# Optimization experiments

Measured on AMD Instinct MI355X. Metric: run time of the kernel, lower is better.

Reference implementation:

```python
import jax, jax.numpy as jnp
import numpy as np

B, T, D, H = 256, 1024, 128, 128

def setup_inputs() -> dict:
    key = jax.random.key(0)
    k1, k2, k3, k4 = jax.random.split(key, 4)
    return {
        "x": jax.random.normal(k1, (B, T, D), dtype=jnp.float32),
        "w": jax.random.normal(k2, (D, H), dtype=jnp.float32) * 0.05,
        "state_weight": jax.random.normal(k3, (H, H), dtype=jnp.float32) * 0.05,
        "b": jax.random.normal(k4, (H,), dtype=jnp.float32) * 0.05,
    }

def reference(x, w, state_weight, b):
    # Faithful Elman RNN with return_sequences=False.
    # Original transposes input to time-major [T, B, D], initializes the
    # state from step 0 WITHOUT a recurrent term, then iterates steps 1..T-1.
    X = jnp.transpose(x, (1, 0, 2))  # [T, B, D]
    # Precompute input projections for all steps in one big GEMM (same math).
    proj = jnp.einsum("tbd,dh->tbh", X, w) + b  # [T, B, H]
    state0 = jnp.tanh(proj[0])

    def step(state, pt):
        y = jnp.tanh(pt + state @ state_weight)
        return y, None

    final_state, _ = jax.lax.scan(step, state0, proj[1:])
    return final_state  # [B, H]
```

## Files before the change

### kernel.cpp

```cpp
#include <hip/hip_runtime.h>

#define T_N 1024
#define H_N 128
#define CH   64
#define NCH (T_N / CH)
#define WPAD 136
#define PPAD 68

typedef __attribute__((ext_vector_type(8))) short bf16x8;
typedef __attribute__((ext_vector_type(4))) float f32x4;

__device__ __forceinline__ short f2bf_rne(float f) {
    union { float f; unsigned int i; } v; v.f = f;
    unsigned int r = v.i + 0x7FFFu + ((v.i >> 16) & 1u);
    return (short)(r >> 16);
}

__global__ __launch_bounds__(512, 1) void k_fused(const float* __restrict__ x,
                                                  const float* __restrict__ w,
                                                  const float* __restrict__ wst,
                                                  const float* __restrict__ bias,
                                                  float* __restrict__ out) {
    __shared__ __align__(16) short wT[H_N * WPAD];
    __shared__ __align__(16) float pT[H_N * PPAD];
    __shared__ __align__(16) short sst[2][H_N];

    const int tid  = threadIdx.x;
    const int wv   = tid >> 6;
    const int lane = tid & 63;
    const int l = lane & 15;
    const int q = lane >> 4;
    const int tt = wv >> 1;
    const int h  = wv & 1;
    const int r = blockIdx.x;
    const float* xrow = x + (size_t)r * T_N * H_N;
    const f32x4 zero4 = (f32x4){0.f, 0.f, 0.f, 0.f};

    const float* xlane = xrow + (size_t)(tt * 16 + l) * H_N + q * 8;
    float4 xst[8];
    #pragma unroll
    for (int ks = 0; ks < 4; ++ks) {
        xst[ks * 2 + 0] = *reinterpret_cast<const float4*>(xlane + ks * 32);
        xst[ks * 2 + 1] = *reinterpret_cast<const float4*>(xlane + ks * 32 + 4);
    }

    short* wsTs = reinterpret_cast<short*>(pT);
    for (int e = tid * 4; e < H_N * H_N; e += 2048) {
        int k = e >> 7, n = e & 127;
        float4 a4 = *reinterpret_cast<const float4*>(wst + e);
        wsTs[(n + 0) * WPAD + k] = f2bf_rne(a4.x);
        wsTs[(n + 1) * WPAD + k] = f2bf_rne(a4.y);
        wsTs[(n + 2) * WPAD + k] = f2bf_rne(a4.z);
        wsTs[(n + 3) * WPAD + k] = f2bf_rne(a4.w);
    }
    __syncthreads();

    bf16x8 wf[4];
    #pragma unroll
    for (int ks = 0; ks < 4; ++ks)
        wf[ks] = *reinterpret_cast<const bf16x8*>(
            &wsTs[(16 * wv + l) * WPAD + ks * 32 + q * 8]);

    if (tid < 128) sst[0][tid] = 0;

    for (int e = tid * 4; e < H_N * H_N; e += 2048) {
        int k = e >> 7, n = e & 127;
        float4 a4 = *reinterpret_cast<const float4*>(w + e);
        wT[(n + 0) * WPAD + k] = f2bf_rne(a4.x);
        wT[(n + 1) * WPAD + k] = f2bf_rne(a4.y);
        wT[(n + 2) * WPAD + k] = f2bf_rne(a4.z);
        wT[(n + 3) * WPAD + k] = f2bf_rne(a4.w);
    }

    float bv[4];
    #pragma unroll
    for (int j = 0; j < 4; ++j) bv[j] = bias[(4 * h + j) * 16 + l];

    __syncthreads();

    float y = 0.f;
    const int rowp = (16 * wv + l) * PPAD;

    auto step = [&](const short* srd, short* swr, float pv) {
        bf16x8 a0 = *reinterpret_cast<const bf16x8*>(&srd[ 0 + q * 8]);
        bf16x8 a1 = *reinterpret_cast<const bf16x8*>(&srd[32 + q * 8]);
        bf16x8 a2 = *reinterpret_cast<const bf16x8*>(&srd[64 + q * 8]);
        bf16x8 a3 = *reinterpret_cast<const bf16x8*>(&srd[96 + q * 8]);
        f32x4 c4 = (f32x4){pv, pv, pv, pv};
        f32x4 x0 = __builtin_amdgcn_mfma_f32_16x16x32_bf16(a0, wf[0], c4, 0, 0, 0);
        f32x4 x1 = __builtin_amdgcn_mfma_f32_16x16x32_bf16(a1, wf[1], zero4, 0, 0, 0);
        f32x4 x2 = __builtin_amdgcn_mfma_f32_16x16x32_bf16(a2, wf[2], zero4, 0, 0, 0);
        f32x4 x3 = __builtin_amdgcn_mfma_f32_16x16x32_bf16(a3, wf[3], zero4, 0, 0, 0);
        float z = (x0[0] + x1[0]) + (x2[0] + x3[0]);
        float e = __expf(2.0f * z);
        y = __builtin_fmaf(-2.0f, __builtin_amdgcn_rcpf(e + 1.0f), 1.0f);
        unsigned int pk;
        asm("v_cvt_pk_bf16_f32 %0, %1, %2" : "=v"(pk) : "v"(y), "v"(y));
        if (q == 0)
            swr[16 * wv + l] = (short)pk;
        __syncthreads();
    };

    #pragma unroll 1
    for (int c = 0; c < NCH; ++c) {
        bf16x8 ax[4];
        #pragma unroll
        for (int ks = 0; ks < 4; ++ks) {
            float4 u0 = xst[ks * 2 + 0];
            float4 u1 = xst[ks * 2 + 1];
            bf16x8 f;
            f[0] = f2bf_rne(u0.x); f[1] = f2bf_rne(u0.y);
            f[2] = f2bf_rne(u0.z); f[3] = f2bf_rne(u0.w);
            f[4] = f2bf_rne(u1.x); f[5] = f2bf_rne(u1.y);
            f[6] = f2bf_rne(u1.z); f[7] = f2bf_rne(u1.w);
            ax[ks] = f;
        }

        if (c + 1 < NCH) {
            const float* pn = xlane + (size_t)(c + 1) * CH * H_N;
            #pragma unroll
            for (int ks = 0; ks < 4; ++ks) {
                xst[ks * 2 + 0] = *reinterpret_cast<const float4*>(pn + ks * 32);
                xst[ks * 2 + 1] = *reinterpret_cast<const float4*>(pn + ks * 32 + 4);
            }
        }


        #pragma unroll
        for (int j = 0; j < 4; ++j) {
            const int nt = 4 * h + j;
            f32x4 cb = (f32x4){bv[j], bv[j], bv[j], bv[j]};
            f32x4 acc;
            #pragma unroll
            for (int ks = 0; ks < 4; ++ks) {
                bf16x8 bw = *reinterpret_cast<const bf16x8*>(
                    &wT[(nt * 16 + l) * WPAD + ks * 32 + q * 8]);
                acc = __builtin_amdgcn_mfma_f32_16x16x32_bf16(
                    ax[ks], bw, ks == 0 ? cb : acc, 0, 0, 0);
            }
            *reinterpret_cast<f32x4*>(&pT[(nt * 16 + l) * PPAD + tt * 16 + q * 4]) = acc;
        }

        __syncthreads();

        #pragma unroll 1
        for (int s = 0; s < CH / 8; ++s) {
            float4 pb0 = *reinterpret_cast<const float4*>(&pT[rowp + 8 * s]);
            float4 pb1 = *reinterpret_cast<const float4*>(&pT[rowp + 8 * s + 4]);
            step(sst[0], sst[1], pb0.x);
            step(sst[1], sst[0], pb0.y);
            step(sst[0], sst[1], pb0.z);
            step(sst[1], sst[0], pb0.w);
            step(sst[0], sst[1], pb1.x);
            step(sst[1], sst[0], pb1.y);
            step(sst[0], sst[1], pb1.z);
            step(sst[1], sst[0], pb1.w);
        }
    }

    if (q == 0)
        out[r * H_N + 16 * wv + l] = y;
}

extern "C" void kernel_launch(void* const* d_in, const int* in_sizes, int n_in,
                              void* d_out, int out_size, void* d_ws, size_t ws_size,
                              hipStream_t stream) {
    const float* x    = (const float*)d_in[0];
    const float* w    = (const float*)d_in[1];
    const float* wst  = (const float*)d_in[2];
    const float* bias = (const float*)d_in[3];
    float* out = (float*)d_out;

    k_fused<<<256, 512, 0, stream>>>(x, w, wst, bias, out);
}
```

Before: 374.2 us.

## Pack two batch rows per 1024-thread block to share weight staging

Each block now runs two independent batch-row recurrences in 1024 threads, organised as two 512-thread groups. Each group gets its own projection buffer and state buffers, while the bf16 input-weight tile is staged in shared memory once per block. The grid is halved to 128 blocks. This means fewer CUs are in use and the block-wide barriers per time step now synchronise both recurrences together. In return, each SIMD may be able to interleave two latency-bound chains.

```diff
diff --git a/kernel.cpp b/kernel.cpp
--- a/kernel.cpp
+++ b/kernel.cpp
@@ -16,24 +16,26 @@
     return (short)(r >> 16);
 }
 
-__global__ __launch_bounds__(512, 1) void k_fused(const float* __restrict__ x,
-                                                  const float* __restrict__ w,
-                                                  const float* __restrict__ wst,
-                                                  const float* __restrict__ bias,
-                                                  float* __restrict__ out) {
+__global__ __launch_bounds__(1024, 1) void k_fused(const float* __restrict__ x,
+                                                   const float* __restrict__ w,
+                                                   const float* __restrict__ wst,
+                                                   const float* __restrict__ bias,
+                                                   float* __restrict__ out) {
     __shared__ __align__(16) short wT[H_N * WPAD];
-    __shared__ __align__(16) float pT[H_N * PPAD];
-    __shared__ __align__(16) short sst[2][H_N];
+    __shared__ __align__(16) float pT[2][H_N * PPAD];
+    __shared__ __align__(16) short sst[2][2][H_N];
 
     const int tid  = threadIdx.x;
-    const int wv   = tid >> 6;
+    const int grp  = tid >> 9;
+    const int wg   = (tid >> 6) & 7;
     const int lane = tid & 63;
     const int l = lane & 15;
     const int q = lane >> 4;
-    const int tt = wv >> 1;
-    const int h  = wv & 1;
-    const int r = blockIdx.x;
+    const int tt = wg >> 1;
+    const int h  = wg & 1;
+    const int r = blockIdx.x * 2 + grp;
     const float* xrow = x + (size_t)r * T_N * H_N;
+    float* pTg = pT[grp];
     const f32x4 zero4 = (f32x4){0.f, 0.f, 0.f, 0.f};
 
     const float* xlane = xrow + (size_t)(tt * 16 + l) * H_N + q * 8;
@@ -44,8 +46,8 @@
         xst[ks * 2 + 1] = *reinterpret_cast<const float4*>(xlane + ks * 32 + 4);
     }
 
-    short* wsTs = reinterpret_cast<short*>(pT);
-    for (int e = tid * 4; e < H_N * H_N; e += 2048) {
+    short* wsTs = reinterpret_cast<short*>(&pT[0][0]);
+    for (int e = tid * 4; e < H_N * H_N; e += 4096) {
         int k = e >> 7, n = e & 127;
         float4 a4 = *reinterpret_cast<const float4*>(wst + e);
         wsTs[(n + 0) * WPAD + k] = f2bf_rne(a4.x);
@@ -59,11 +61,14 @@
     #pragma unroll
     for (int ks = 0; ks < 4; ++ks)
         wf[ks] = *reinterpret_cast<const bf16x8*>(
-            &wsTs[(16 * wv + l) * WPAD + ks * 32 + q * 8]);
+            &wsTs[(16 * wg + l) * WPAD + ks * 32 + q * 8]);
 
-    if (tid < 128) sst[0][tid] = 0;
+    {
+        int gt = tid & 511;
+        if (gt < 128) sst[grp][0][gt] = 0;
+    }
 
-    for (int e = tid * 4; e < H_N * H_N; e += 2048) {
+    for (int e = tid * 4; e < H_N * H_N; e += 4096) {
         int k = e >> 7, n = e & 127;
         float4 a4 = *reinterpret_cast<const float4*>(w + e);
         wT[(n + 0) * WPAD + k] = f2bf_rne(a4.x);
@@ -79,7 +84,7 @@
     __syncthreads();
 
     float y = 0.f;
-    const int rowp = (16 * wv + l) * PPAD;
+    const int rowp = (16 * wg + l) * PPAD;
 
     auto step = [&](const short* srd, short* swr, float pv) {
         bf16x8 a0 = *reinterpret_cast<const bf16x8*>(&srd[ 0 + q * 8]);
@@ -97,7 +102,7 @@
         unsigned int pk;
         asm("v_cvt_pk_bf16_f32 %0, %1, %2" : "=v"(pk) : "v"(y), "v"(y));
         if (q == 0)
-            swr[16 * wv + l] = (short)pk;
+            swr[16 * wg + l] = (short)pk;
         __syncthreads();
     };
 
@@ -138,28 +143,30 @@
                 acc = __builtin_amdgcn_mfma_f32_16x16x32_bf16(
                     ax[ks], bw, ks == 0 ? cb : acc, 0, 0, 0);
             }
-            *reinterpret_cast<f32x4*>(&pT[(nt * 16 + l) * PPAD + tt * 16 + q * 4]) = acc;
+            *reinterpret_cast<f32x4*>(&pTg[(nt * 16 + l) * PPAD + tt * 16 + q * 4]) = acc;
         }
 
         __syncthreads();
 
+        short* s0 = sst[grp][0];
+        short* s1 = sst[grp][1];
         #pragma unroll 1
         for (int s = 0; s < CH / 8; ++s) {
-            float4 pb0 = *reinterpret_cast<const float4*>(&pT[rowp + 8 * s]);
-            float4 pb1 = *reinterpret_cast<const float4*>(&pT[rowp + 8 * s + 4]);
-            step(sst[0], sst[1], pb0.x);
-            step(sst[1], sst[0], pb0.y);
-            step(sst[0], sst[1], pb0.z);
-            step(sst[1], sst[0], pb0.w);
-            step(sst[0], sst[1], pb1.x);
-            step(sst[1], sst[0], pb1.y);
-            step(sst[0], sst[1], pb1.z);
-            step(sst[1], sst[0], pb1.w);
+            float4 pb0 = *reinterpret_cast<const float4*>(&pTg[rowp + 8 * s]);
+            float4 pb1 = *reinterpret_cast<const float4*>(&pTg[rowp + 8 * s + 4]);
+            step(s0, s1, pb0.x);
+            step(s1, s0, pb0.y);
+            step(s0, s1, pb0.z);
+            step(s1, s0, pb0.w);
+            step(s0, s1, pb1.x);
+            step(s1, s0, pb1.y);
+            step(s0, s1, pb1.z);
+            step(s1, s0, pb1.w);
         }
     }
 
     if (q == 0)
-        out[r * H_N + 16 * wv + l] = y;
+        out[r * H_N + 16 * wg + l] = y;
 }
 
 extern "C" void kernel_launch(void* const* d_in, const int* in_sizes, int n_in,
@@ -171,5 +178,5 @@
     const float* bias = (const float*)d_in[3];
     float* out = (float*)d_out;
 
-    k_fused<<<256, 512, 0, stream>>>(x, w, wst, bias, out);
+    k_fused<<<128, 1024, 0, stream>>>(x, w, wst, bias, out);
 }
```

Result: slower. 487.1 us (+30.2%).
